# Kernel tuning notes

Hardware: AMD Instinct MI355X
Metric: run time of the kernel (lower is better)

The kernel has to match this reference:

```python
import jax, jax.numpy as jnp
import numpy as np

B, S, H = 1, 4096, 2048
NH, NKV = 16, 4
HD = H // NH  # 128
GROUPS = NH // NKV


def setup_inputs() -> dict:
    key = jax.random.key(0)
    ks = jax.random.split(key, 5)
    hidden_states = jax.random.normal(ks[0], (B, S, H), dtype=jnp.float32)
    # causal additive mask: 0 on/below diagonal, large negative above
    neg = jnp.finfo(jnp.float32).min
    causal = jnp.where(jnp.tril(jnp.ones((S, S), dtype=bool)), 0.0, neg)
    attention_mask = jnp.broadcast_to(causal, (B, 1, S, S)).astype(jnp.float32)
    sc = 0.02
    Wq = jax.random.normal(ks[1], (H, NH * HD), dtype=jnp.float32) * sc
    Wk = jax.random.normal(ks[2], (H, NKV * HD), dtype=jnp.float32) * sc
    Wv = jax.random.normal(ks[3], (H, NKV * HD), dtype=jnp.float32) * sc
    Wo = jax.random.normal(ks[4], (H, H), dtype=jnp.float32) * sc
    return {"hidden_states": hidden_states, "attention_mask": attention_mask,
            "Wq": Wq, "Wk": Wk, "Wv": Wv, "Wo": Wo}


def reference(hidden_states, attention_mask, Wq, Wk, Wv, Wo):
    b, s, _ = hidden_states.shape
    # projections -> (b, heads, s, hd)
    q = (hidden_states @ Wq).reshape(b, s, NH, HD).transpose(0, 2, 1, 3)
    k = (hidden_states @ Wk).reshape(b, s, NKV, HD).transpose(0, 2, 1, 3)
    v = (hidden_states @ Wv).reshape(b, s, NKV, HD).transpose(0, 2, 1, 3)
    # repeat_kv for GQA: (b, nkv, s, hd) -> (b, nh, s, hd)
    k = jnp.repeat(k, GROUPS, axis=1)
    v = jnp.repeat(v, GROUPS, axis=1)
    scores = jnp.einsum('bhqd,bhkd->bhqk', q, k) / jnp.sqrt(jnp.float32(HD))
    scores = scores + attention_mask
    attn = jax.nn.softmax(scores.astype(jnp.float32), axis=-1).astype(q.dtype)
    out = jnp.einsum('bhqk,bhkd->bhqd', attn, v)
    out = out.transpose(0, 2, 1, 3).reshape(b, s, H)
    return out @ Wo
```

## Files before the change

kernel.cpp:

```cpp
#include <hip/hip_runtime.h>


typedef __bf16 bf16;
typedef float f32x4 __attribute__((ext_vector_type(4)));
typedef float f32x16 __attribute__((ext_vector_type(16)));
typedef bf16 bf16x4 __attribute__((ext_vector_type(4)));
typedef bf16 bf16x8 __attribute__((ext_vector_type(8)));
typedef unsigned u32x4 __attribute__((ext_vector_type(4)));

#define MFMA16(A, B, C) __builtin_amdgcn_mfma_f32_16x16x32_bf16((A), (B), (C), 0, 0, 0)
#define MFMA32(A, B, C) __builtin_amdgcn_mfma_f32_32x32x16_bf16((A), (B), (C), 0, 0, 0)

__device__ __forceinline__ void async16(const bf16* g, bf16* l) {
  __builtin_amdgcn_global_load_lds(
      (const __attribute__((address_space(1))) unsigned int*)g,
      (__attribute__((address_space(3))) unsigned int*)l, 16, 0, 0);
}

__device__ __forceinline__ float exp2v(float x) {
  float r; asm("v_exp_f32 %0, %1" : "=v"(r) : "v"(x)); return r;
}
__device__ __forceinline__ unsigned cvtpk(float a, float b) {
  unsigned r; asm("v_cvt_pk_bf16_f32 %0, %1, %2" : "=v"(r) : "v"(a), "v"(b)); return r;
}
#define PLSWAP(a, b) asm("v_permlane32_swap_b32 %0, %1" : "+v"(a), "+v"(b))

__device__ __forceinline__ bf16x8 mkfrag(unsigned a0, unsigned a1,
                                         unsigned c0, unsigned c1) {
  PLSWAP(a0, c0);
  PLSWAP(a1, c1);
  u32x4 t = {a0, a1, c0, c1};
  return __builtin_bit_cast(bf16x8, t);
}

__global__ void cast_bf16_kernel(const float* __restrict__ in,
                                 bf16* __restrict__ out, int n4) {
  int i = blockIdx.x * blockDim.x + threadIdx.x;
  int stride = gridDim.x * blockDim.x;
  for (; i < n4; i += stride) {
    float4 v = ((const float4*)in)[i];
    bf16x4 o = {(bf16)v.x, (bf16)v.y, (bf16)v.z, (bf16)v.w};
    ((bf16x4*)out)[i] = o;
  }
}

__global__ void transpose_cast_kernel(const float* __restrict__ src, int srcCols,
                                      bf16* __restrict__ dst, float scale) {
  __shared__ float t[64][65];
  const int kt = blockIdx.y * 64;
  const int nt = blockIdx.x * 64;
  const int r0 = threadIdx.x >> 4;
  const int c0 = (threadIdx.x & 15) * 4;
#pragma unroll
  for (int i = 0; i < 4; ++i) {
    int r = r0 + i * 16;
    float4 v = *(const float4*)(src + (kt + r) * srcCols + nt + c0);
    t[r][c0 + 0] = v.x; t[r][c0 + 1] = v.y; t[r][c0 + 2] = v.z; t[r][c0 + 3] = v.w;
  }
  __syncthreads();
#pragma unroll
  for (int i = 0; i < 4; ++i) {
    int r = r0 + i * 16;
    bf16x4 b = {(bf16)(t[c0 + 0][r] * scale), (bf16)(t[c0 + 1][r] * scale),
                (bf16)(t[c0 + 2][r] * scale), (bf16)(t[c0 + 3][r] * scale)};
    *(bf16x4*)(dst + (nt + r) * 2048 + kt + c0) = b;
  }
}

template <int MODE>
__global__ __launch_bounds__(256, 2) void gemm_bt(
    const bf16* __restrict__ A, const bf16* __restrict__ BT, int K,
    bf16* __restrict__ Qb, bf16* __restrict__ Kb, bf16* __restrict__ Vt,
    float* __restrict__ Cf) {
  __shared__ bf16 As[128 * 32];
  __shared__ bf16 Bs[128 * 32];
  const int tid = threadIdx.x;
  const int w = tid >> 6, lane = tid & 63, g = lane >> 4, lq = lane & 15;
  const int wr = w >> 1, wc = w & 1;
  const int mBase = blockIdx.y * 128, nBase = blockIdx.x * 128;

  f32x4 acc[4][4] = {};
  const int KT = K >> 5;
  for (int kt = 0; kt < KT; ++kt) {
#pragma unroll
    for (int r = 0; r < 2; ++r) {
      int chunk = r * 256 + tid;
      int row = chunk >> 2, cu = chunk & 3;
      async16(A + (mBase + row) * K + kt * 32 + cu * 8, As + (r * 256 + w * 64) * 8);
      async16(BT + (nBase + row) * K + kt * 32 + cu * 8, Bs + (r * 256 + w * 64) * 8);
    }
    asm volatile("s_waitcnt vmcnt(0)" ::: "memory");
    __syncthreads();

    bf16x8 af[4], bfr[4];
#pragma unroll
    for (int i = 0; i < 4; ++i)
      af[i] = *(const bf16x8*)(As + (wr * 64 + i * 16 + lq) * 32 + g * 8);
#pragma unroll
    for (int i = 0; i < 4; ++i)
      bfr[i] = *(const bf16x8*)(Bs + (wc * 64 + i * 16 + lq) * 32 + g * 8);
#pragma unroll
    for (int mi = 0; mi < 4; ++mi)
#pragma unroll
      for (int ni = 0; ni < 4; ++ni)
        acc[mi][ni] = MFMA16(af[mi], bfr[ni], acc[mi][ni]);
    __syncthreads();
  }

#pragma unroll
  for (int mi = 0; mi < 4; ++mi)
#pragma unroll
    for (int ni = 0; ni < 4; ++ni) {
      const int n = nBase + wc * 64 + ni * 16 + lq;
      const int m0 = mBase + wr * 64 + mi * 16 + 4 * g;
      if (MODE == 0) {
        if (nBase < 2048) {
#pragma unroll
          for (int jr = 0; jr < 4; ++jr)
            Qb[(m0 + jr) * 2048 + n] = (bf16)acc[mi][ni][jr];
        } else if (nBase < 2560) {
#pragma unroll
          for (int jr = 0; jr < 4; ++jr)
            Kb[(m0 + jr) * 512 + (n - 2048)] = (bf16)acc[mi][ni][jr];
        } else {
          bf16x4 v = {(bf16)acc[mi][ni][0], (bf16)acc[mi][ni][1],
                      (bf16)acc[mi][ni][2], (bf16)acc[mi][ni][3]};
          *(bf16x4*)(Vt + (n - 2560) * 4096 + m0) = v;
        }
      } else {
#pragma unroll
        for (int jr = 0; jr < 4; ++jr)
          Cf[(m0 + jr) * 2048 + n] = acc[mi][ni][jr];
      }
    }
}

__global__ __launch_bounds__(256, 2) void attn_fwd(
    const bf16* __restrict__ Qb,
    const bf16* __restrict__ Kb,
    const bf16* __restrict__ Vt,
    bf16* __restrict__ AO) {
  __shared__ __align__(16) bf16 Ks[2][64 * 128];
  __shared__ __align__(16) bf16 Vs[2][128 * 64];

  const int bid = blockIdx.x;
  const int h = bid & 15;
  const int qt = (bid < 256) ? (bid >> 4) : (31 - ((bid - 256) >> 4));
  const int kv = h >> 2;
  const int tid = threadIdx.x;
  const int w = tid >> 6, lane = tid & 63, l5 = lane & 31, g2 = lane >> 5;
  const int sxr = (l5 & 7) << 4;
  const int qbase = qt * 128;
  const int nk = 2 * (qt + 1);
  const int qw = qbase + w * 32 + l5;

  bf16x8 aq[8];
  {
    const bf16* qrow = Qb + qw * 2048 + h * 128;
#pragma unroll
    for (int kk = 0; kk < 8; ++kk)
      aq[kk] = *(const bf16x8*)(qrow + kk * 16 + g2 * 8);
  }

  float mst = -1e30f, lst = 0.f;
  f32x16 o[4] = {};

  auto STAGE = [&](int t) {
    const int b = t & 1;
#pragma unroll
    for (int r = 0; r < 4; ++r) {
      int gid = r * 256 + tid;
      int krow = gid >> 4, cu = gid & 15;
      async16(Kb + (t * 64 + krow) * 512 + kv * 128 + ((cu ^ (krow & 7)) * 8),
              &Ks[b][(r * 256 + w * 64) * 8]);
    }
#pragma unroll
    for (int r = 0; r < 4; ++r) {
      int gid = r * 256 + tid;
      int vrow = gid >> 3, gv = gid & 7;
      async16(Vt + (kv * 128 + vrow) * 4096 + t * 64 + ((gv ^ (vrow & 7)) * 8),
              &Vs[b][(r * 256 + w * 64) * 8]);
    }
  };

  STAGE(0);

  for (int t = 0; t < nk; ++t) {
    const int cur = t & 1;
    if (t + 1 < nk) {
      STAGE(t + 1);
      asm volatile("s_waitcnt vmcnt(8)" ::: "memory");
    } else {
      asm volatile("s_waitcnt vmcnt(0)" ::: "memory");
    }
    __builtin_amdgcn_s_barrier();
    __builtin_amdgcn_sched_barrier(0);

    f32x16 s0 = {}, s1 = {};
    {
      const char* kb0 = (const char*)&Ks[cur][0] + l5 * 256;
      __builtin_amdgcn_s_setprio(1);
#pragma unroll
      for (int kk = 0; kk < 8; ++kk) {
        const int off = (kk * 32 + g2 * 16) ^ sxr;
        bf16x8 k0 = *(const bf16x8*)(kb0 + off);
        bf16x8 k1 = *(const bf16x8*)(kb0 + 8192 + off);
        s0 = MFMA32(k0, aq[kk], s0);
        s1 = MFMA32(k1, aq[kk], s1);
      }
      __builtin_amdgcn_s_setprio(0);
    }

    if (t >= 2 * qt) {
      const int kb = t * 64 + 4 * g2;
#pragma unroll
      for (int r = 0; r < 16; ++r) {
        const int key = kb + (r & 3) + 8 * (r >> 2);
        if (key > qw) s0[r] = -1e30f;
        if (key + 32 > qw) s1[r] = -1e30f;
      }
    }

    {
      float mx[16];
#pragma unroll
      for (int r = 0; r < 16; ++r) mx[r] = fmaxf(s0[r], s1[r]);
#pragma unroll
      for (int off = 8; off > 0; off >>= 1)
#pragma unroll
        for (int r = 0; r < off; ++r) mx[r] = fmaxf(mx[r], mx[r + off]);
      const float pm = fmaxf(mx[0], __shfl_xor(mx[0], 32));

      if (__any(pm > mst + 8.f)) {
        const float mn = fmaxf(mst, pm);
        const float al = exp2v(mst - mn);
        mst = mn;
        lst *= al;
#pragma unroll
        for (int dt = 0; dt < 4; ++dt)
#pragma unroll
          for (int r = 0; r < 16; ++r) o[dt][r] *= al;
      }
#pragma unroll
      for (int r = 0; r < 16; ++r) {
        s0[r] = exp2v(s0[r] - mst);
        s1[r] = exp2v(s1[r] - mst);
      }
      float sm[16];
#pragma unroll
      for (int r = 0; r < 16; ++r) sm[r] = s0[r] + s1[r];
#pragma unroll
      for (int off = 8; off > 0; off >>= 1)
#pragma unroll
        for (int r = 0; r < off; ++r) sm[r] += sm[r + off];
      lst += sm[0] + __shfl_xor(sm[0], 32);
    }

    unsigned pw0[8], pw1[8];
#pragma unroll
    for (int wi = 0; wi < 8; ++wi) {
      pw0[wi] = cvtpk(s0[2 * wi], s0[2 * wi + 1]);
      pw1[wi] = cvtpk(s1[2 * wi], s1[2 * wi + 1]);
    }
    bf16x8 pb0 = mkfrag(pw0[0], pw0[1], pw0[2], pw0[3]);
    bf16x8 pb1 = mkfrag(pw0[4], pw0[5], pw0[6], pw0[7]);
    bf16x8 pb2 = mkfrag(pw1[0], pw1[1], pw1[2], pw1[3]);
    bf16x8 pb3 = mkfrag(pw1[4], pw1[5], pw1[6], pw1[7]);

    {
      __builtin_amdgcn_s_setprio(1);
#pragma unroll
      for (int dt = 0; dt < 4; ++dt) {
        const char* vb = (const char*)&Vs[cur][0] + (dt * 32 + l5) * 128;
        bf16x8 av;
        av = *(const bf16x8*)(vb + ((0 * 32 + g2 * 16) ^ sxr));
        o[dt] = MFMA32(av, pb0, o[dt]);
        av = *(const bf16x8*)(vb + ((1 * 32 + g2 * 16) ^ sxr));
        o[dt] = MFMA32(av, pb1, o[dt]);
        av = *(const bf16x8*)(vb + ((2 * 32 + g2 * 16) ^ sxr));
        o[dt] = MFMA32(av, pb2, o[dt]);
        av = *(const bf16x8*)(vb + ((3 * 32 + g2 * 16) ^ sxr));
        o[dt] = MFMA32(av, pb3, o[dt]);
      }
      __builtin_amdgcn_s_setprio(0);
    }

    __builtin_amdgcn_sched_barrier(0);
    __builtin_amdgcn_s_barrier();
  }

  {
    const float inv = 1.f / lst;
    bf16* aob = AO + qw * 2048 + h * 128;
#pragma unroll
    for (int dt = 0; dt < 4; ++dt)
#pragma unroll
      for (int m = 0; m < 4; ++m) {
        bf16x4 ov = {(bf16)(o[dt][4 * m + 0] * inv), (bf16)(o[dt][4 * m + 1] * inv),
                     (bf16)(o[dt][4 * m + 2] * inv), (bf16)(o[dt][4 * m + 3] * inv)};
        *(bf16x4*)(aob + dt * 32 + 8 * m + 4 * g2) = ov;
      }
  }
}

extern "C" void kernel_launch(void* const* d_in, const int* in_sizes, int n_in,
                              void* d_out, int out_size, void* d_ws, size_t ws_size,
                              hipStream_t stream) {
  const float* X = (const float*)d_in[0];
  const float* Wq = (const float*)d_in[2];
  const float* Wk = (const float*)d_in[3];
  const float* Wv = (const float*)d_in[4];
  const float* Wo = (const float*)d_in[5];
  float* out = (float*)d_out;
  char* ws = (char*)d_ws;

  bf16* Xb = (bf16*)ws;
  bf16* WT = (bf16*)(ws + 16777216);
  bf16* Qb = (bf16*)(ws + 29360128);
  bf16* Kb = (bf16*)(ws + 46137344);
  bf16* Vt = (bf16*)(ws + 50331648);

  cast_bf16_kernel<<<2048, 256, 0, stream>>>(X, Xb, (4096 * 2048) / 4);
  transpose_cast_kernel<<<dim3(32, 32), 256, 0, stream>>>(
      Wq, 2048, WT, 0.08838834764831845f * 1.4426950408889634f);
  transpose_cast_kernel<<<dim3(8, 32), 256, 0, stream>>>(Wk, 512, WT + 2048 * 2048, 1.0f);
  transpose_cast_kernel<<<dim3(8, 32), 256, 0, stream>>>(Wv, 512, WT + 2560 * 2048, 1.0f);

  gemm_bt<0><<<dim3(24, 32), 256, 0, stream>>>(Xb, WT, 2048, Qb, Kb, Vt, (float*)nullptr);

  transpose_cast_kernel<<<dim3(32, 32), 256, 0, stream>>>(Wo, 2048, WT, 1.0f);

  attn_fwd<<<512, 256, 0, stream>>>(Qb, Kb, Vt, Xb);

  gemm_bt<1><<<dim3(16, 32), 256, 0, stream>>>(Xb, WT, 2048, (bf16*)nullptr,
                                               (bf16*)nullptr, (bf16*)nullptr, out);
}
```

Baseline: 263.2 us.

## Software-pipeline QK^T of next tile with PV of current tile in attention

Restructures the flash-attention loop so the QK^T MFMAs for the next key tile are interleaved with the PV MFMAs for the current tile. K and V loads are staged separately, with K prefetched two tiles ahead and V one tile ahead, and there is a prologue that computes the first score tile. The intent is to hide the softmax and exp latency and LDS reads behind independent matrix work. It costs extra live registers for the next-tile accumulators, which may reduce occupancy or cause spills. The redundant loads issued on the last iterations also complicate the vmcnt accounting.

```diff
diff --git a/kernel.cpp b/kernel.cpp
--- a/kernel.cpp
+++ b/kernel.cpp
@@ -165,51 +165,51 @@
   float mst = -1e30f, lst = 0.f;
   f32x16 o[4] = {};
 
-  auto STAGE = [&](int t) {
-    const int b = t & 1;
+  auto STAGE_K = [&](int t, int buf) {
 #pragma unroll
     for (int r = 0; r < 4; ++r) {
       int gid = r * 256 + tid;
       int krow = gid >> 4, cu = gid & 15;
       async16(Kb + (t * 64 + krow) * 512 + kv * 128 + ((cu ^ (krow & 7)) * 8),
-              &Ks[b][(r * 256 + w * 64) * 8]);
-    }
+              &Ks[buf][(r * 256 + w * 64) * 8]);
+    }
+  };
+  auto STAGE_V = [&](int t, int buf) {
 #pragma unroll
     for (int r = 0; r < 4; ++r) {
       int gid = r * 256 + tid;
       int vrow = gid >> 3, gv = gid & 7;
       async16(Vt + (kv * 128 + vrow) * 4096 + t * 64 + ((gv ^ (vrow & 7)) * 8),
-              &Vs[b][(r * 256 + w * 64) * 8]);
+              &Vs[buf][(r * 256 + w * 64) * 8]);
     }
   };
 
-  STAGE(0);
+  STAGE_K(0, 0);
+  STAGE_V(0, 0);
+  STAGE_K(1, 1);
+  asm volatile("s_waitcnt vmcnt(8)" ::: "memory");
+  __builtin_amdgcn_s_barrier();
+  __builtin_amdgcn_sched_barrier(0);
+
+  f32x16 s0 = {}, s1 = {};
+  {
+    const char* kb0 = (const char*)&Ks[0][0] + l5 * 256;
+    __builtin_amdgcn_s_setprio(1);
+#pragma unroll
+    for (int kk = 0; kk < 8; ++kk) {
+      const int off = (kk * 32 + g2 * 16) ^ sxr;
+      bf16x8 k0 = *(const bf16x8*)(kb0 + off);
+      bf16x8 k1 = *(const bf16x8*)(kb0 + 8192 + off);
+      s0 = MFMA32(k0, aq[kk], s0);
+      s1 = MFMA32(k1, aq[kk], s1);
+    }
+    __builtin_amdgcn_s_setprio(0);
+  }
+  __builtin_amdgcn_sched_barrier(0);
+  __builtin_amdgcn_s_barrier();
 
   for (int t = 0; t < nk; ++t) {
-    const int cur = t & 1;
-    if (t + 1 < nk) {
-      STAGE(t + 1);
-      asm volatile("s_waitcnt vmcnt(8)" ::: "memory");
-    } else {
-      asm volatile("s_waitcnt vmcnt(0)" ::: "memory");
-    }
-    __builtin_amdgcn_s_barrier();
-    __builtin_amdgcn_sched_barrier(0);
-
-    f32x16 s0 = {}, s1 = {};
-    {
-      const char* kb0 = (const char*)&Ks[cur][0] + l5 * 256;
-      __builtin_amdgcn_s_setprio(1);
-#pragma unroll
-      for (int kk = 0; kk < 8; ++kk) {
-        const int off = (kk * 32 + g2 * 16) ^ sxr;
-        bf16x8 k0 = *(const bf16x8*)(kb0 + off);
-        bf16x8 k1 = *(const bf16x8*)(kb0 + 8192 + off);
-        s0 = MFMA32(k0, aq[kk], s0);
-        s1 = MFMA32(k1, aq[kk], s1);
-      }
-      __builtin_amdgcn_s_setprio(0);
-    }
+    const int cur = t & 1, nxt = (t + 1) & 1;
 
     if (t >= 2 * qt) {
       const int kb = t * 64 + 4 * g2;
@@ -256,37 +256,68 @@
       lst += sm[0] + __shfl_xor(sm[0], 32);
     }
 
-    unsigned pw0[8], pw1[8];
-#pragma unroll
-    for (int wi = 0; wi < 8; ++wi) {
-      pw0[wi] = cvtpk(s0[2 * wi], s0[2 * wi + 1]);
-      pw1[wi] = cvtpk(s1[2 * wi], s1[2 * wi + 1]);
-    }
-    bf16x8 pb0 = mkfrag(pw0[0], pw0[1], pw0[2], pw0[3]);
-    bf16x8 pb1 = mkfrag(pw0[4], pw0[5], pw0[6], pw0[7]);
-    bf16x8 pb2 = mkfrag(pw1[0], pw1[1], pw1[2], pw1[3]);
-    bf16x8 pb3 = mkfrag(pw1[4], pw1[5], pw1[6], pw1[7]);
-
+    bf16x8 pb[4];
     {
+      unsigned pw0[8], pw1[8];
+#pragma unroll
+      for (int wi = 0; wi < 8; ++wi) {
+        pw0[wi] = cvtpk(s0[2 * wi], s0[2 * wi + 1]);
+        pw1[wi] = cvtpk(s1[2 * wi], s1[2 * wi + 1]);
+      }
+      pb[0] = mkfrag(pw0[0], pw0[1], pw0[2], pw0[3]);
+      pb[1] = mkfrag(pw0[4], pw0[5], pw0[6], pw0[7]);
+      pb[2] = mkfrag(pw1[0], pw1[1], pw1[2], pw1[3]);
+      pb[3] = mkfrag(pw1[4], pw1[5], pw1[6], pw1[7]);
+    }
+
+    STAGE_K(min(t + 2, nk - 1), cur);
+    STAGE_V(min(t + 1, nk - 1), nxt);
+    asm volatile("s_waitcnt vmcnt(8)" ::: "memory");
+    __builtin_amdgcn_s_barrier();
+    __builtin_amdgcn_sched_barrier(0);
+
+    f32x16 n0 = {}, n1 = {};
+    const char* kb0 = (const char*)&Ks[nxt][0] + l5 * 256;
+    const char* vb0 = (const char*)&Vs[cur][0];
+    if (t + 1 < nk) {
       __builtin_amdgcn_s_setprio(1);
 #pragma unroll
-      for (int dt = 0; dt < 4; ++dt) {
-        const char* vb = (const char*)&Vs[cur][0] + (dt * 32 + l5) * 128;
-        bf16x8 av;
-        av = *(const bf16x8*)(vb + ((0 * 32 + g2 * 16) ^ sxr));
-        o[dt] = MFMA32(av, pb0, o[dt]);
-        av = *(const bf16x8*)(vb + ((1 * 32 + g2 * 16) ^ sxr));
-        o[dt] = MFMA32(av, pb1, o[dt]);
-        av = *(const bf16x8*)(vb + ((2 * 32 + g2 * 16) ^ sxr));
-        o[dt] = MFMA32(av, pb2, o[dt]);
-        av = *(const bf16x8*)(vb + ((3 * 32 + g2 * 16) ^ sxr));
-        o[dt] = MFMA32(av, pb3, o[dt]);
+      for (int i = 0; i < 8; ++i) {
+        const int koff = (i * 32 + g2 * 16) ^ sxr;
+        bf16x8 k0 = *(const bf16x8*)(kb0 + koff);
+        bf16x8 k1 = *(const bf16x8*)(kb0 + 8192 + koff);
+        n0 = MFMA32(k0, aq[i], n0);
+        n1 = MFMA32(k1, aq[i], n1);
+        {
+          const int j = 2 * i, dt = j & 3, KK = j >> 2;
+          bf16x8 av = *(const bf16x8*)(vb0 + (dt * 32 + l5) * 128 +
+                                       ((KK * 32 + g2 * 16) ^ sxr));
+          o[dt] = MFMA32(av, pb[KK], o[dt]);
+        }
+        {
+          const int j = 2 * i + 1, dt = j & 3, KK = j >> 2;
+          bf16x8 av = *(const bf16x8*)(vb0 + (dt * 32 + l5) * 128 +
+                                       ((KK * 32 + g2 * 16) ^ sxr));
+          o[dt] = MFMA32(av, pb[KK], o[dt]);
+        }
       }
       __builtin_amdgcn_s_setprio(0);
-    }
-
+    } else {
+      __builtin_amdgcn_s_setprio(1);
+#pragma unroll
+      for (int j = 0; j < 16; ++j) {
+        const int dt = j & 3, KK = j >> 2;
+        bf16x8 av = *(const bf16x8*)(vb0 + (dt * 32 + l5) * 128 +
+                                     ((KK * 32 + g2 * 16) ^ sxr));
+        o[dt] = MFMA32(av, pb[KK], o[dt]);
+      }
+      __builtin_amdgcn_s_setprio(0);
+    }
     __builtin_amdgcn_sched_barrier(0);
     __builtin_amdgcn_s_barrier();
+
+    s0 = n0;
+    s1 = n1;
   }
 
   {
```

Result: faster. 258.0 us (-2.0%).
